# Kernel tuning notes

Hardware: AMD Instinct MI355X
Metric: run time of the kernel (lower is better)

## Reference

```python
import jax, jax.numpy as jnp
import numpy as np

N = 65536      # n query/support points
NN = 34        # neighbors per point
K = 15         # kernel points
IN_F = 64
OUT_F = 64
RADIUS = 2.5
KP_EXTENT_CFG = 1.0
DENSITY = 5.0
EXTENT = KP_EXTENT_CFG * RADIUS / DENSITY  # effective KP_extent = 0.5
BN_EPS = 1e-6
LRELU_SLOPE = 0.1
POINT_DIM = 4  # modulated=True -> 3 offset dims + 1 modulation per kernel point


def make_kernel_points():
    # Deterministic stand-in for the precomputed kernel dispositions loaded
    # from disk in KPConv (fixed='center': first point at origin). Points lie
    # inside a ball of radius 1.5 * extent.
    rng = np.random.RandomState(42)
    kp = rng.normal(size=(K, 3))
    kp /= np.linalg.norm(kp, axis=1, keepdims=True)
    kp *= rng.uniform(0.3, 1.0, size=(K, 1))
    kp[0] = 0.0
    return jnp.asarray(kp * (1.5 * EXTENT), dtype=jnp.float32)


def setup_inputs() -> dict:
    key = jax.random.key(0)
    ks = jax.random.split(key, 8)
    query_points = jax.random.uniform(ks[0], (N, 3), dtype=jnp.float32)
    support_points = jax.random.uniform(ks[1], (N, 3), dtype=jnp.float32)
    neighbors_indices = jax.random.randint(ks[2], (N, NN), 0, N, dtype=jnp.int32)
    features = jax.random.normal(ks[3], (N, IN_F), dtype=jnp.float32)
    # weight_variable: truncated normal with std sqrt(2/size[-1])
    weight = jax.random.truncated_normal(ks[4], -2.0, 2.0, (K, IN_F, OUT_F), jnp.float32) * np.sqrt(2.0 / OUT_F)
    off_dim = POINT_DIM * K
    offset_weight = jax.random.truncated_normal(ks[5], -2.0, 2.0, (K, IN_F, off_dim), jnp.float32) * np.sqrt(2.0 / off_dim)
    offset_bias = jnp.zeros((off_dim,), jnp.float32)
    bn_gamma = jnp.ones((OUT_F,), jnp.float32)
    bn_beta = jnp.zeros((OUT_F,), jnp.float32)
    kernel_points = make_kernel_points()
    return dict(query_points=query_points, support_points=support_points,
                neighbors_indices=neighbors_indices, features=features,
                weight=weight, offset_weight=offset_weight, offset_bias=offset_bias,
                bn_gamma=bn_gamma, bn_beta=bn_beta, kernel_points=kernel_points)


def _influence(sq_dist):
    # KP_influence='linear': relu(1 - d / extent)
    return jax.nn.relu(1.0 - jnp.sqrt(sq_dist) / EXTENT)


def reference(query_points, support_points, neighbors_indices, features,
              weight, offset_weight, offset_bias, bn_gamma, bn_beta, kernel_points):
    n = query_points.shape[0]
    # Shadow point (far away) / shadow feature (zeros) appended at index n0
    supp_pad = jnp.concatenate([support_points, jnp.full((1, 3), 1e6, jnp.float32)], 0)
    feat_pad = jnp.concatenate([features, jnp.zeros((1, IN_F), jnp.float32)], 0)

    neigh_pts = supp_pad[neighbors_indices] - query_points[:, None, :]   # [n,nn,3]
    neigh_feats = feat_pad[neighbors_indices]                            # [n,nn,in]

    # ---- rigid KPConv producing per-point offsets (+ modulations) ----
    sq0 = jnp.sum((neigh_pts[:, :, None, :] - kernel_points[None, None]) ** 2, -1)  # [n,nn,K]
    w0 = _influence(sq0)
    wf0 = jnp.einsum('nak,nac->nkc', w0, neigh_feats)                    # [n,K,in]
    f0 = jnp.einsum('nkc,kcd->nd', wf0, offset_weight) + offset_bias     # [n,4K]
    offsets = f0[:, :3 * K].reshape(n, K, 3) * EXTENT                    # rescale to layer extent
    modulations = 2.0 * jax.nn.sigmoid(f0[:, 3 * K:])                    # [n,K]

    # ---- deformable KPConv ----
    def_kp = kernel_points[None] + offsets                               # [n,K,3]
    sq = jnp.sum((neigh_pts[:, :, None, :] - def_kp[:, None, :, :]) ** 2, -1)  # [n,nn,K]
    w = _influence(sq)                                                   # aggregation_mode='sum'
    wf = jnp.einsum('nak,nac->nkc', w, neigh_feats) * modulations[:, :, None]
    x = jnp.einsum('nkc,kco->no', wf, weight)                            # [n,out]

    # BatchNorm1d (training-mode batch stats, eps=1e-6) + LeakyReLU(0.1)
    mean = x.mean(0)
    var = x.var(0)
    x = (x - mean) * jax.lax.rsqrt(var + BN_EPS) * bn_gamma + bn_beta
    return jnp.where(x >= 0, x, LRELU_SLOPE * x)
```

## Files before the change

### kernel.cpp

```cpp
#include <hip/hip_runtime.h>
#include <math.h>

#define NPTS 65536

using half8   = __attribute__((ext_vector_type(8))) _Float16;
using half4   = __attribute__((ext_vector_type(4))) _Float16;
using floatx4 = __attribute__((ext_vector_type(4))) float;

__global__ __launch_bounds__(256) void k_prep(
    const float* __restrict__ ow, const float* __restrict__ w,
    const float* __restrict__ feat,
    _Float16* __restrict__ owt, _Float16* __restrict__ wt,
    _Float16* __restrict__ featH, float* __restrict__ stats)
{
  int b = blockIdx.x;
  if (b < 256) {
    int i = b * 256 + threadIdx.x;
    int d = i >> 10, kc = i & 1023, c = kc >> 4, k = kc & 15;
    owt[i] = (k < 15 && d < 60) ? (_Float16)ow[(k * 64 + c) * 60 + d] : (_Float16)0.f;
    wt[i]  = (k < 15) ? (_Float16)w[(k * 64 + c) * 64 + d] : (_Float16)0.f;
    if (b == 0 && threadIdx.x < 128) stats[threadIdx.x] = 0.f;
  } else {
    int j = (b - 256) * 256 + threadIdx.x;
    float4 f = ((const float4*)feat)[j];
    half4 h = {(_Float16)f.x, (_Float16)f.y, (_Float16)f.z, (_Float16)f.w};
    ((half4*)featH)[j] = h;
  }
}

__global__ __launch_bounds__(256, 3) void k_fused(
    const float* __restrict__ query, const float* __restrict__ support,
    const int* __restrict__ nidx, const _Float16* __restrict__ featH,
    const float* __restrict__ kpts, const float* __restrict__ obias,
    const _Float16* __restrict__ owt, const _Float16* __restrict__ wt,
    float* __restrict__ outx, float* __restrict__ stats)
{
  __shared__ float                  npx[16][34], npy[16][34], npz[16][34];
  __shared__ unsigned short         sidx[16][34];
  __shared__ __align__(16) _Float16 fT[4][64 * 32];
  __shared__ unsigned int           fx2[4][64];
  __shared__ __align__(16) _Float16 wfh[16 * 264];
  __shared__ float                  dk[16][60];

  const int tid  = threadIdx.x;
  const int wave = tid >> 6, lane = tid & 63;
  const int quad = lane >> 4, mm = lane & 15;
  const int base = blockIdx.x * 16;
  _Float16* fTw = fT[wave];
  unsigned int* fTw32 = (unsigned int*)fTw;
  unsigned int* fx2w = fx2[wave];
  const floatx4 fz = {0.f, 0.f, 0.f, 0.f};
  const int me = (mm < 15) ? mm : 14;

  for (int s = tid; s < 544; s += 256) {
    int pt = s / 34, a = s - pt * 34;
    int n = base + pt;
    int id = nidx[n * 34 + a];
    npx[pt][a] = support[id * 3 + 0] - query[n * 3 + 0];
    npy[pt][a] = support[id * 3 + 1] - query[n * 3 + 1];
    npz[pt][a] = support[id * 3 + 2] - query[n * 3 + 2];
    sidx[pt][a] = (unsigned short)id;
  }
  __syncthreads();

  auto load_g = [&](int pl, uint4* g0, uint4* g1) {
    #pragma unroll
    for (int it = 0; it < 3; ++it) {
      int task = it * 64 + lane;
      if (task < 136) {
        int rp = task >> 3, ch = task & 7;
        int i0 = (int)sidx[pl][2 * rp], i1 = (int)sidx[pl][2 * rp + 1];
        g0[it] = *(const uint4*)(featH + i0 * 64 + ch * 8);
        g1[it] = *(const uint4*)(featH + i1 * 64 + ch * 8);
      }
    }
  };
  auto transpose_g = [&](const uint4* g0, const uint4* g1) {
    #pragma unroll
    for (int it = 0; it < 3; ++it) {
      int task = it * 64 + lane;
      if (task < 136) {
        int rp = task >> 3, ch = task & 7;
        const uint* p0 = (const uint*)&g0[it];
        const uint* p1 = (const uint*)&g1[it];
        if (rp < 16) {
          int chunk = rp >> 2, o = rp & 3;
          #pragma unroll
          for (int cc = 0; cc < 8; ++cc) {
            int c  = ch * 8 + cc;
            int pc = chunk ^ ((ch ^ cc) & 3);
            uint v = __builtin_amdgcn_perm(p1[cc >> 1], p0[cc >> 1],
                                           (cc & 1) ? 0x07060302u : 0x05040100u);
            fTw32[c * 16 + pc * 4 + o] = v;
          }
        } else {
          #pragma unroll
          for (int cc = 0; cc < 8; ++cc) {
            uint v = __builtin_amdgcn_perm(p1[cc >> 1], p0[cc >> 1],
                                           (cc & 1) ? 0x07060302u : 0x05040100u);
            fx2w[ch * 8 + cc] = v;
          }
        }
      }
    }
  };

  auto conv_point = [&](int pl, float kx, float ky, float kz, float modme,
                        half4* hq) {
    half8 a0;
    #pragma unroll
    for (int j = 0; j < 8; ++j) {
      int a = quad * 8 + j;
      float dx = npx[pl][a] - kx, dy = npy[pl][a] - ky, dz = npz[pl][a] - kz;
      float wv = 1.f - 2.f * sqrtf(dx * dx + dy * dy + dz * dz);
      a0[j] = (_Float16)(fmaxf(wv, 0.f) * modme);
    }
    float dx = npx[pl][32] - kx, dy = npy[pl][32] - ky, dz = npz[pl][32] - kz;
    float w32 = fmaxf(1.f - 2.f * sqrtf(dx * dx + dy * dy + dz * dz), 0.f) * modme;
    dx = npx[pl][33] - kx; dy = npy[pl][33] - ky; dz = npz[pl][33] - kz;
    float w33 = fmaxf(1.f - 2.f * sqrtf(dx * dx + dy * dy + dz * dz), 0.f) * modme;
    half8 a2 = {};
    a2[0] = (_Float16)((quad == 0) ? w32 : 0.f);
    a2[1] = (_Float16)((quad == 0) ? w33 : 0.f);
    #pragma unroll
    for (int ct = 0; ct < 4; ++ct) {
      int c  = ct * 16 + mm;
      int pc = quad ^ (((c >> 3) ^ c) & 3);
      half8 b = *(const half8*)(fTw + c * 32 + pc * 8);
      floatx4 acc = __builtin_amdgcn_mfma_f32_16x16x32_f16(a0, b, fz, 0, 0, 0);
      uint fp = fx2w[c];
      half8 b2 = {};
      b2[0] = __builtin_bit_cast(_Float16, (unsigned short)(fp & 0xffffu));
      b2[1] = __builtin_bit_cast(_Float16, (unsigned short)(fp >> 16));
      acc = __builtin_amdgcn_mfma_f32_16x16x32_f16(a2, b2, acc, 0, 0, 0);
      half4 h = {(_Float16)acc[0], (_Float16)acc[1],
                 (_Float16)acc[2], (_Float16)acc[3]};
      if (ct == 0) *(half4*)(wfh + pl * 264 + mm * 16 + quad * 4) = h;
      else         hq[ct - 1] = h;
    }
  };

  auto write_hold = [&](const half4 (*hq)[3], int idx) {
    #pragma unroll
    for (int pp = 0; pp < 4; ++pp)
      *(half4*)(wfh + (wave * 4 + pp) * 264 + mm * 16 + quad * 4) = hq[pp][idx];
  };

  auto gemm_q = [&](const _Float16* bmat, int p, floatx4& A, floatx4& B) {
    const _Float16* brow = bmat + (wave * 16 + mm) * 1024 + p * 256;
    const _Float16* arow = wfh + mm * 264;
    #pragma unroll
    for (int k2 = 0; k2 < 8; ++k2) {
      half8 af = *(const half8*)(arow + k2 * 32 + quad * 8);
      half8 bf = *(const half8*)(brow + k2 * 32 + quad * 8);
      if (k2 & 1) B = __builtin_amdgcn_mfma_f32_16x16x32_f16(af, bf, B, 0, 0, 0);
      else        A = __builtin_amdgcn_mfma_f32_16x16x32_f16(af, bf, A, 0, 0, 0);
    }
  };

  uint4 G0[2][3], G1[2][3];
  half4 hq[4][3];
  const float k0x = kpts[me * 3 + 0], k0y = kpts[me * 3 + 1], k0z = kpts[me * 3 + 2];

  {
    load_g(wave * 4, G0[0], G1[0]);
    #pragma unroll
    for (int pp = 0; pp < 4; ++pp) {
      int pl = wave * 4 + pp;
      if (pp < 3) load_g(pl + 1, G0[(pp + 1) & 1], G1[(pp + 1) & 1]);
      transpose_g(G0[pp & 1], G1[pp & 1]);
      conv_point(pl, k0x, k0y, k0z, 1.f, hq[pp]);
    }
  }
  load_g(wave * 4, G0[0], G1[0]);
  __syncthreads();

  {
    floatx4 A = fz, B = fz;
    gemm_q(owt, 0, A, B);
    __syncthreads(); write_hold(hq, 0); __syncthreads();
    gemm_q(owt, 1, A, B);
    __syncthreads(); write_hold(hq, 1); __syncthreads();
    gemm_q(owt, 2, A, B);
    __syncthreads(); write_hold(hq, 2); __syncthreads();
    gemm_q(owt, 3, A, B);
    int d = wave * 16 + mm;
    float bv = (d < 60) ? obias[d] : 0.f;
    float kv = (d < 45) ? kpts[d] : 0.f;
    #pragma unroll
    for (int r = 0; r < 4; ++r) {
      int pt = quad * 4 + r;
      float v = A[r] + B[r] + bv;
      if (d < 60)
        dk[pt][d] = (d < 45) ? (kv + 0.5f * v)
                             : (2.f / (1.f + expf(-v)));
    }
  }
  __syncthreads();

  #pragma unroll
  for (int pp = 0; pp < 4; ++pp) {
    int pl = wave * 4 + pp;
    if (pp < 3) load_g(pl + 1, G0[(pp + 1) & 1], G1[(pp + 1) & 1]);
    float kx = dk[pl][me * 3 + 0], ky = dk[pl][me * 3 + 1], kz = dk[pl][me * 3 + 2];
    float modme = dk[pl][45 + me];
    transpose_g(G0[pp & 1], G1[pp & 1]);
    conv_point(pl, kx, ky, kz, modme, hq[pp]);
  }
  __syncthreads();

  {
    floatx4 A = fz, B = fz;
    gemm_q(wt, 0, A, B);
    __syncthreads(); write_hold(hq, 0); __syncthreads();
    gemm_q(wt, 1, A, B);
    __syncthreads(); write_hold(hq, 1); __syncthreads();
    gemm_q(wt, 2, A, B);
    __syncthreads(); write_hold(hq, 2); __syncthreads();
    gemm_q(wt, 3, A, B);
    int d = wave * 16 + mm;
    float s1 = 0.f, s2 = 0.f;
    #pragma unroll
    for (int r = 0; r < 4; ++r) {
      float v = A[r] + B[r];
      outx[(base + quad * 4 + r) * 64 + d] = v;
      s1 += v; s2 += v * v;
    }
    s1 += __shfl_xor(s1, 16); s2 += __shfl_xor(s2, 16);
    s1 += __shfl_xor(s1, 32); s2 += __shfl_xor(s2, 32);
    if (lane < 16) {
      atomicAdd(&stats[d], s1);
      atomicAdd(&stats[64 + d], s2);
    }
  }
}

__global__ __launch_bounds__(256) void k_norm(
    float* __restrict__ x, const float* __restrict__ stats,
    const float* __restrict__ gamma, const float* __restrict__ beta)
{
  const int i = blockIdx.x * 256 + threadIdx.x;
  float4 v = ((float4*)x)[i];
  const int c0 = (i * 4) & 63;
  float o[4] = {v.x, v.y, v.z, v.w};
  #pragma unroll
  for (int j = 0; j < 4; ++j) {
    int c = c0 + j;
    float mean = stats[c] * (1.f / NPTS);
    float var  = stats[64 + c] * (1.f / NPTS) - mean * mean;
    float s = rsqrtf(var + 1e-6f) * gamma[c];
    float y = (o[j] - mean) * s + beta[c];
    o[j] = (y >= 0.f) ? y : 0.1f * y;
  }
  float4 rv = {o[0], o[1], o[2], o[3]};
  ((float4*)x)[i] = rv;
}

extern "C" void kernel_launch(void* const* d_in, const int* in_sizes, int n_in,
                              void* d_out, int out_size, void* d_ws, size_t ws_size,
                              hipStream_t stream)
{
  const float* query   = (const float*)d_in[0];
  const float* support = (const float*)d_in[1];
  const int*   nidx    = (const int*)d_in[2];
  const float* feat    = (const float*)d_in[3];
  const float* weight  = (const float*)d_in[4];
  const float* oweight = (const float*)d_in[5];
  const float* obias   = (const float*)d_in[6];
  const float* gamma   = (const float*)d_in[7];
  const float* beta    = (const float*)d_in[8];
  const float* kpts    = (const float*)d_in[9];
  float* x = (float*)d_out;

  char* ws = (char*)d_ws;
  _Float16* featH = (_Float16*)ws;
  _Float16* owt   = (_Float16*)(ws + 8388608);
  _Float16* wt    = (_Float16*)(ws + 8519680);
  float*    stats = (float*)(ws + 8650752);

  k_prep<<<4352, 256, 0, stream>>>(oweight, weight, feat, owt, wt, featH, stats);
  k_fused<<<4096, 256, 0, stream>>>(query, support, nidx, featH, kpts, obias,
                                    owt, wt, x, stats);
  k_norm<<<4096, 256, 0, stream>>>(x, stats, gamma, beta);
}
```

Before: 297.1 us.

## Precompute tail-neighbor features once in shared memory and raise occupancy target

```diff
diff --git a/kernel.cpp b/kernel.cpp
--- a/kernel.cpp
+++ b/kernel.cpp
@@ -28,7 +28,7 @@
   }
 }
 
-__global__ __launch_bounds__(256, 3) void k_fused(
+__global__ __launch_bounds__(256, 4) void k_fused(
     const float* __restrict__ query, const float* __restrict__ support,
     const int* __restrict__ nidx, const _Float16* __restrict__ featH,
     const float* __restrict__ kpts, const float* __restrict__ obias,
@@ -38,7 +38,7 @@
   __shared__ float                  npx[16][34], npy[16][34], npz[16][34];
   __shared__ unsigned short         sidx[16][34];
   __shared__ __align__(16) _Float16 fT[4][64 * 32];
-  __shared__ unsigned int           fx2[4][64];
+  __shared__ unsigned int           fx2s[16][64];
   __shared__ __align__(16) _Float16 wfh[16 * 264];
   __shared__ float                  dk[16][60];
 
@@ -48,7 +48,6 @@
   const int base = blockIdx.x * 16;
   _Float16* fTw = fT[wave];
   unsigned int* fTw32 = (unsigned int*)fTw;
-  unsigned int* fx2w = fx2[wave];
   const floatx4 fz = {0.f, 0.f, 0.f, 0.f};
   const int me = (mm < 15) ? mm : 14;
 
@@ -63,50 +62,53 @@
   }
   __syncthreads();
 
+  if (tid < 128) {
+    int pt = tid >> 3, ch = tid & 7;
+    int i0 = (int)sidx[pt][32], i1 = (int)sidx[pt][33];
+    uint4 g0 = *(const uint4*)(featH + i0 * 64 + ch * 8);
+    uint4 g1 = *(const uint4*)(featH + i1 * 64 + ch * 8);
+    const uint* p0 = (const uint*)&g0;
+    const uint* p1 = (const uint*)&g1;
+    #pragma unroll
+    for (int cc = 0; cc < 8; ++cc) {
+      uint v = __builtin_amdgcn_perm(p1[cc >> 1], p0[cc >> 1],
+                                     (cc & 1) ? 0x07060302u : 0x05040100u);
+      fx2s[pt][ch * 8 + cc] = v;
+    }
+  }
+  __syncthreads();
+
   auto load_g = [&](int pl, uint4* g0, uint4* g1) {
     #pragma unroll
-    for (int it = 0; it < 3; ++it) {
+    for (int it = 0; it < 2; ++it) {
       int task = it * 64 + lane;
-      if (task < 136) {
-        int rp = task >> 3, ch = task & 7;
-        int i0 = (int)sidx[pl][2 * rp], i1 = (int)sidx[pl][2 * rp + 1];
-        g0[it] = *(const uint4*)(featH + i0 * 64 + ch * 8);
-        g1[it] = *(const uint4*)(featH + i1 * 64 + ch * 8);
+      int rp = task >> 3, ch = task & 7;
+      int i0 = (int)sidx[pl][2 * rp], i1 = (int)sidx[pl][2 * rp + 1];
+      g0[it] = *(const uint4*)(featH + i0 * 64 + ch * 8);
+      g1[it] = *(const uint4*)(featH + i1 * 64 + ch * 8);
+    }
+  };
+  auto transpose_g = [&](const uint4* g0, const uint4* g1) {
+    #pragma unroll
+    for (int it = 0; it < 2; ++it) {
+      int task = it * 64 + lane;
+      int rp = task >> 3, ch = task & 7;
+      int chunk = rp >> 2, o = rp & 3;
+      const uint* p0 = (const uint*)&g0[it];
+      const uint* p1 = (const uint*)&g1[it];
+      #pragma unroll
+      for (int cc = 0; cc < 8; ++cc) {
+        int c  = ch * 8 + cc;
+        int pc = chunk ^ ((ch ^ cc) & 3);
+        uint v = __builtin_amdgcn_perm(p1[cc >> 1], p0[cc >> 1],
+                                       (cc & 1) ? 0x07060302u : 0x05040100u);
+        fTw32[c * 16 + pc * 4 + o] = v;
       }
     }
   };
-  auto transpose_g = [&](const uint4* g0, const uint4* g1) {
-    #pragma unroll
-    for (int it = 0; it < 3; ++it) {
-      int task = it * 64 + lane;
-      if (task < 136) {
-        int rp = task >> 3, ch = task & 7;
-        const uint* p0 = (const uint*)&g0[it];
-        const uint* p1 = (const uint*)&g1[it];
-        if (rp < 16) {
-          int chunk = rp >> 2, o = rp & 3;
-          #pragma unroll
-          for (int cc = 0; cc < 8; ++cc) {
-            int c  = ch * 8 + cc;
-            int pc = chunk ^ ((ch ^ cc) & 3);
-            uint v = __builtin_amdgcn_perm(p1[cc >> 1], p0[cc >> 1],
-                                           (cc & 1) ? 0x07060302u : 0x05040100u);
-            fTw32[c * 16 + pc * 4 + o] = v;
-          }
-        } else {
-          #pragma unroll
-          for (int cc = 0; cc < 8; ++cc) {
-            uint v = __builtin_amdgcn_perm(p1[cc >> 1], p0[cc >> 1],
-                                           (cc & 1) ? 0x07060302u : 0x05040100u);
-            fx2w[ch * 8 + cc] = v;
-          }
-        }
-      }
-    }
-  };
 
   auto conv_point = [&](int pl, float kx, float ky, float kz, float modme,
-                        half4* hq) {
+                        half4* hq3) {
     half8 a0;
     #pragma unroll
     for (int j = 0; j < 8; ++j) {
@@ -128,7 +130,7 @@
       int pc = quad ^ (((c >> 3) ^ c) & 3);
       half8 b = *(const half8*)(fTw + c * 32 + pc * 8);
       floatx4 acc = __builtin_amdgcn_mfma_f32_16x16x32_f16(a0, b, fz, 0, 0, 0);
-      uint fp = fx2w[c];
+      uint fp = fx2s[pl][c];
       half8 b2 = {};
       b2[0] = __builtin_bit_cast(_Float16, (unsigned short)(fp & 0xffffu));
       b2[1] = __builtin_bit_cast(_Float16, (unsigned short)(fp >> 16));
@@ -136,7 +138,7 @@
       half4 h = {(_Float16)acc[0], (_Float16)acc[1],
                  (_Float16)acc[2], (_Float16)acc[3]};
       if (ct == 0) *(half4*)(wfh + pl * 264 + mm * 16 + quad * 4) = h;
-      else         hq[ct - 1] = h;
+      else         hq3[ct - 1] = h;
     }
   };
 
@@ -158,21 +160,21 @@
     }
   };
 
-  uint4 G0[2][3], G1[2][3];
+  uint4 G0[2], G1[2];
   half4 hq[4][3];
   const float k0x = kpts[me * 3 + 0], k0y = kpts[me * 3 + 1], k0z = kpts[me * 3 + 2];
 
   {
-    load_g(wave * 4, G0[0], G1[0]);
+    load_g(wave * 4, G0, G1);
     #pragma unroll
     for (int pp = 0; pp < 4; ++pp) {
       int pl = wave * 4 + pp;
-      if (pp < 3) load_g(pl + 1, G0[(pp + 1) & 1], G1[(pp + 1) & 1]);
-      transpose_g(G0[pp & 1], G1[pp & 1]);
+      transpose_g(G0, G1);
+      if (pp < 3) load_g(pl + 1, G0, G1);
       conv_point(pl, k0x, k0y, k0z, 1.f, hq[pp]);
     }
   }
-  load_g(wave * 4, G0[0], G1[0]);
+  load_g(wave * 4, G0, G1);
   __syncthreads();
 
   {
@@ -201,10 +203,10 @@
   #pragma unroll
   for (int pp = 0; pp < 4; ++pp) {
     int pl = wave * 4 + pp;
-    if (pp < 3) load_g(pl + 1, G0[(pp + 1) & 1], G1[(pp + 1) & 1]);
     float kx = dk[pl][me * 3 + 0], ky = dk[pl][me * 3 + 1], kz = dk[pl][me * 3 + 2];
     float modme = dk[pl][45 + me];
-    transpose_g(G0[pp & 1], G1[pp & 1]);
+    transpose_g(G0, G1);
+    if (pp < 3) load_g(pl + 1, G0, G1);
     conv_point(pl, kx, ky, kz, modme, hq[pp]);
   }
   __syncthreads();
```

Measured after the change: 287.5 us. 3.2% less time.
